# Performance work log

Measured on AMD Instinct MI355X. Metric: run time of the kernel, lower is better.

## Reference

```python
import jax, jax.numpy as jnp
import numpy as np

B, S = 16, 128
P, M, H = 512, 64, 256
I = P + M            # LTC input dim = perception + metadata
U = 2 * H            # ncp_units = hidden_dim * 2
OUT = 64             # belief head output size
UNFOLDS = 6          # ncps LTC default ode_unfolds
HEADS = 4
DH = H // HEADS


def setup_inputs() -> dict:
    key = jax.random.key(0)
    ks = jax.random.split(key, 24)
    u = lambda k, sh, lo, hi: jax.random.uniform(k, sh, jnp.float32, lo, hi)
    sgn = lambda k, sh: jnp.where(jax.random.bernoulli(k, 0.5, sh), 1.0, -1.0).astype(jnp.float32)
    msk = lambda k, sh: jax.random.bernoulli(k, 0.6, sh).astype(jnp.float32)
    gl = lambda k, sh, s: jax.random.normal(k, sh, jnp.float32) * s
    return dict(
        x=jax.random.normal(ks[0], (B, S, I), jnp.float32),
        # ncps LTC affine input/output maps (init: w=1, b=0)
        input_w=jnp.ones((I,), jnp.float32), input_b=jnp.zeros((I,), jnp.float32),
        # LTC cell params, ncps init ranges
        gleak=u(ks[1], (U,), 0.001, 1.0), vleak=u(ks[2], (U,), -0.2, 0.2),
        cm=u(ks[3], (U,), 0.4, 0.6),
        sigma=u(ks[4], (U, U), 3.0, 8.0), mu=u(ks[5], (U, U), 0.3, 0.8),
        w=u(ks[6], (U, U), 0.001, 1.0), erev=sgn(ks[7], (U, U)),
        sparsity_mask=msk(ks[8], (U, U)),  # AutoNCP sparse wiring surrogate
        sensory_sigma=u(ks[9], (I, U), 3.0, 8.0), sensory_mu=u(ks[10], (I, U), 0.3, 0.8),
        sensory_w=u(ks[11], (I, U), 0.001, 1.0), sensory_erev=sgn(ks[12], (I, U)),
        sensory_sparsity_mask=msk(ks[13], (I, U)),
        output_w=jnp.ones((H,), jnp.float32), output_b=jnp.zeros((H,), jnp.float32),
        # Hopfield (multi-head associative retrieval) projections
        Wq=gl(ks[14], (H, H), H ** -0.5), bq=jnp.zeros((H,), jnp.float32),
        Wk=gl(ks[15], (H, H), H ** -0.5), bk=jnp.zeros((H,), jnp.float32),
        Wv=gl(ks[16], (H, H), H ** -0.5), bv=jnp.zeros((H,), jnp.float32),
        Wo=gl(ks[17], (H, H), H ** -0.5), bo=jnp.zeros((H,), jnp.float32),
        # belief head
        W1=gl(ks[18], (H, H), H ** -0.5), b1=jnp.zeros((H,), jnp.float32),
        W2=gl(ks[19], (H, OUT), H ** -0.5), b2=jnp.zeros((OUT,), jnp.float32),
    )


def reference(x, input_w, input_b, gleak, vleak, cm, sigma, mu, w, erev,
              sparsity_mask, sensory_sigma, sensory_mu, sensory_w, sensory_erev,
              sensory_sparsity_mask, output_w, output_b,
              Wq, bq, Wk, bk, Wv, bv, Wo, bo, W1, b1, W2, b2):
    cm_t = cm * UNFOLDS  # cm / (elapsed_time / ode_unfolds), elapsed_time = 1.0

    @jax.checkpoint
    def cell(h, x_t):
        inp = x_t * input_w + input_b  # affine input map
        # sensory synapse activations: (B, I, U)
        sa = sensory_w * jax.nn.sigmoid(sensory_sigma * (inp[:, :, None] - sensory_mu)) * sensory_sparsity_mask
        w_num_s = jnp.sum(sa * sensory_erev, axis=1)  # (B, U)
        w_den_s = jnp.sum(sa, axis=1)
        v = h
        for _ in range(UNFOLDS):  # semi-implicit Euler ODE unfolds
            act = w * jax.nn.sigmoid(sigma * (v[:, :, None] - mu)) * sparsity_mask  # (B, U, U)
            w_num = jnp.sum(act * erev, axis=1) + w_num_s
            w_den = jnp.sum(act, axis=1) + w_den_s
            v = (cm_t * v + gleak * vleak + w_num) / (cm_t + gleak + w_den + 1e-8)
        out = v[:, :H] * output_w + output_b  # motor neurons + affine output map
        return v, out

    h0 = jnp.zeros((x.shape[0], U), x.dtype)
    h, outs = jax.lax.scan(cell, h0, jnp.swapaxes(x, 0, 1))  # outs: (S, B, H)
    ltc_out = jnp.swapaxes(outs, 0, 1)  # (B, S, H)

    # Hopfield associative memory (single update step == MHA self-retrieval)
    q = (ltc_out @ Wq + bq).reshape(B, S, HEADS, DH)
    k = (ltc_out @ Wk + bk).reshape(B, S, HEADS, DH)
    v = (ltc_out @ Wv + bv).reshape(B, S, HEADS, DH)
    attn = jax.nn.softmax(jnp.einsum('bqhd,bkhd->bhqk', q, k) / np.sqrt(DH).astype(np.float32), axis=-1)
    mem = jnp.einsum('bhqk,bkhd->bqhd', attn, v).reshape(B, S, H) @ Wo + bo

    combined = ltc_out + mem
    belief = jax.nn.silu(combined @ W1 + b1) @ W2 + b2
    return combined, belief, h
```

## Files before the change

### kernel.cpp

```cpp
#include <hip/hip_runtime.h>
#include <hip/hip_fp16.h>

#define L2E 1.4426950408889634f

constexpr int Bb = 16, Ss = 128, Ii = 576, Uu = 512, Hh = 256;

constexpr int OFF_AC   = 0;
constexpr int OFF_W2   = 262144;
constexpr int OFF_NUMS = 393216;
constexpr int OFF_DENS = 1441792;
constexpr int OFF_LTC  = 2499072;
constexpr int OFF_Q    = 3023360;
constexpr int OFF_K    = 3547648;
constexpr int OFF_V    = 4071936;
constexpr int OFF_MEM  = 4596224;
constexpr int OFF_HID  = 5120512;

constexpr unsigned SENT_U = 0x7FBADBADu;

__device__ __forceinline__ float ex2(float x) { return __builtin_amdgcn_exp2f(x); }
__device__ __forceinline__ float rcpf(float x) { return __builtin_amdgcn_rcpf(x); }

__global__ __launch_bounds__(256) void prep_kernel(
    const float* __restrict__ sigma, const float* __restrict__ mu,
    const float* __restrict__ w, const float* __restrict__ erev,
    const float* __restrict__ mask, float* __restrict__ ws)
{
    const int t = threadIdx.x;
    {
        const int g = blockIdx.x * 256 + t;
        if (g < 16 * 8 * 512) {
            const int r = (g >> 9) & 7;
            ws[OFF_HID + g] = (r == 7) ? 0.0f : __builtin_bit_cast(float, SENT_U);
        }
    }
    const int p = blockIdx.x * 256 + t;
    const int i2 = p >> 9, jj = p & 511;
    const int slice = jj >> 4, jl = jj & 15;
    unsigned* AC = (unsigned*)ws + OFF_AC;
    unsigned* W2 = (unsigned*)ws + OFF_W2;
    __half weh0, weh1;
    {
        const int i = i2 * 2;
        const int idx = i * 512 + jj;
        const float sg = sigma[idx], m = mu[idx];
        const float wm = w[idx] * mask[idx];
        __half2 ac; ac.x = __float2half_rn(sg * L2E); ac.y = __float2half_rn(sg * m * L2E);
        AC[slice * 8192 + ((i * 16 + jl) ^ (((i >> 5) & 1) << 4))] = __builtin_bit_cast(unsigned, ac);
        weh0 = __float2half_rn(wm * erev[idx]);
    }
    {
        const int i = i2 * 2 + 1;
        const int idx = i * 512 + jj;
        const float sg = sigma[idx], m = mu[idx];
        const float wm = w[idx] * mask[idx];
        __half2 ac; ac.x = __float2half_rn(sg * L2E); ac.y = __float2half_rn(sg * m * L2E);
        AC[slice * 8192 + ((i * 16 + jl) ^ (((i >> 5) & 1) << 4))] = __builtin_bit_cast(unsigned, ac);
        weh1 = __float2half_rn(wm * erev[idx]);
    }
    __half2 wp; wp.x = weh0; wp.y = weh1;
    W2[slice * 4096 + ((i2 * 16 + jl) ^ (((i2 >> 4) & 1) << 4))] = __builtin_bit_cast(unsigned, wp);
}

__global__ __launch_bounds__(256) void sensory_kernel(
    const float* __restrict__ x, const float* __restrict__ inw, const float* __restrict__ inb,
    const float* __restrict__ ssig, const float* __restrict__ smu,
    const float* __restrict__ sw, const float* __restrict__ serev,
    const float* __restrict__ smask, float* __restrict__ ws)
{
    __shared__ float inp[16 * 576];
    __shared__ float part[4096];
    const int t = threadIdx.x;
    const int jb = blockIdx.x & 7, pb = blockIdx.x >> 3;
    #pragma unroll
    for (int e = 0; e < 9; ++e) {
        const int id = t + e * 256;
        const int off = id * 4;
        const int bs = off / 576, ii = off % 576;
        const float4 xv = *(const float4*)&x[(pb * 16 + bs) * 576 + ii];
        const float4 wv = *(const float4*)&inw[ii];
        const float4 bv = *(const float4*)&inb[ii];
        inp[off + 0] = fmaf(xv.x, wv.x, bv.x);
        inp[off + 1] = fmaf(xv.y, wv.y, bv.y);
        inp[off + 2] = fmaf(xv.z, wv.z, bv.z);
        inp[off + 3] = fmaf(xv.w, wv.w, bv.w);
    }
    __syncthreads();
    const int j = t & 63, c = t >> 6;
    const int jg = jb * 64 + j;
    float num[16], den[16];
    #pragma unroll
    for (int bs = 0; bs < 16; ++bs) { num[bs] = 0.f; den[bs] = 0.f; }
    for (int ii = c * 144; ii < (c + 1) * 144; ++ii) {
        const int pidx = ii * 512 + jg;
        const float sg = ssig[pidx], m = smu[pidx];
        const float wm = sw[pidx] * smask[pidx];
        const float we = wm * serev[pidx];
        const float a = sg * L2E, cc = sg * m * L2E;
        #pragma unroll
        for (int bs = 0; bs < 16; ++bs) {
            const float vv = inp[bs * 576 + ii];
            const float r = rcpf(1.f + ex2(fmaf(-a, vv, cc)));
            num[bs] = fmaf(we, r, num[bs]);
            den[bs] = fmaf(wm, r, den[bs]);
        }
    }
    #pragma unroll
    for (int pass = 0; pass < 2; ++pass) {
        __syncthreads();
        #pragma unroll
        for (int bs = 0; bs < 8; ++bs) {
            part[((c * 64 + j) * 8 + bs) * 2 + 0] = num[pass * 8 + bs];
            part[((c * 64 + j) * 8 + bs) * 2 + 1] = den[pass * 8 + bs];
        }
        __syncthreads();
        #pragma unroll
        for (int qd = 0; qd < 4; ++qd) {
            const int vid = t * 4 + qd;
            const int jj2 = vid >> 4, bs = (vid >> 1) & 7, which = vid & 1;
            const float acc =
                part[((0 * 64 + jj2) * 8 + bs) * 2 + which] + part[((1 * 64 + jj2) * 8 + bs) * 2 + which] +
                part[((2 * 64 + jj2) * 8 + bs) * 2 + which] + part[((3 * 64 + jj2) * 8 + bs) * 2 + which];
            const int p = pb * 16 + pass * 8 + bs;
            ws[(which ? OFF_DENS : OFF_NUMS) + p * 512 + jb * 64 + jj2] = acc;
        }
    }
}

__global__ __launch_bounds__(256) void scan_kernel(
    const float* __restrict__ gleak, const float* __restrict__ vleak,
    const float* __restrict__ cmv,
    const float* __restrict__ outw, const float* __restrict__ outb,
    float* __restrict__ ws, float* __restrict__ dout)
{
    __shared__ unsigned prmAC[8192];
    __shared__ unsigned prmW2[4096];
    __shared__ float vlds[512];
    __shared__ float2 red[64];

    const int t = threadIdx.x;
    const int wg = blockIdx.x;
    const int batch = wg & 15;
    const int slice = wg >> 4;
    const int jl = t & 15;
    const int chunk = t >> 4;
    const unsigned swz = (unsigned)((chunk & 1) << 4);

    {
        const uint4* sA = (const uint4*)((const unsigned*)ws + OFF_AC) + slice * 2048;
        uint4* dA = (uint4*)prmAC;
        #pragma unroll
        for (int k = 0; k < 8; ++k) dA[t + k * 256] = sA[t + k * 256];
        const uint4* sW = (const uint4*)((const unsigned*)ws + OFF_W2) + slice * 1024;
        uint4* dW = (uint4*)prmW2;
        #pragma unroll
        for (int k = 0; k < 4; ++k) dW[t + k * 256] = sW[t + k * 256];
    }

    const bool owner = (t < 16);
    const int j = slice * 16 + jl;
    float gl = 0.f, glvl = 0.f, cmt = 0.f, ow = 0.f, ob = 0.f, vown = 0.f, sn = 0.f, sd = 0.f;
    if (owner) {
        gl = gleak[j]; glvl = gl * vleak[j]; cmt = cmv[j] * 6.f;
        if (j < Hh) { ow = outw[j]; ob = outb[j]; }
    }
    float* vb2 = ws + OFF_HID + batch * 4096;
    const float* snb = ws + OFF_NUMS + batch * (Ss * Uu);
    const float* sdb = ws + OFF_DENS + batch * (Ss * Uu);
    float* ltc = ws + OFF_LTC;

    __syncthreads();

    unsigned phase = 0;
    const int ibase = chunk * 32;

    for (int step = 0; step < Ss; ++step) {
        if (owner) { sn = snb[step * Uu + j]; sd = sdb[step * Uu + j]; }
        for (int uf = 0; uf < 6; ++uf) {
            if (owner) {
                __hip_atomic_store(vb2 + (((phase + 4) & 7) << 9) + j,
                                   __builtin_bit_cast(float, SENT_U),
                                   __ATOMIC_RELAXED, __HIP_MEMORY_SCOPE_AGENT);
            }
            {
                const float* src = vb2 + (((phase + 7) & 7) << 9);
                float va = 0.f, vc = 0.f;
                unsigned ua = SENT_U, uc = SENT_U;
                do {
                    if (ua == SENT_U) {
                        va = __hip_atomic_load(src + t, __ATOMIC_RELAXED, __HIP_MEMORY_SCOPE_AGENT);
                        ua = __builtin_bit_cast(unsigned, va);
                    }
                    if (uc == SENT_U) {
                        vc = __hip_atomic_load(src + t + 256, __ATOMIC_RELAXED, __HIP_MEMORY_SCOPE_AGENT);
                        uc = __builtin_bit_cast(unsigned, vc);
                    }
                } while (ua == SENT_U || uc == SENT_U);
                vlds[t] = va; vlds[t + 256] = vc;
            }
            __syncthreads();

            float n0 = 0.f, n1 = 0.f, d0 = 0.f, d1 = 0.f;
            #pragma unroll
            for (int kk = 0; kk < 8; ++kk) {
                const int ib = ibase + kk * 4;
                const float4 v4 = *(const float4*)&vlds[ib];
                const int eb = ib * 16 + jl;
                const int pbi = (ib >> 1) * 16 + jl;
                const unsigned ac0 = prmAC[(unsigned)(eb) ^ swz];
                const unsigned ac1 = prmAC[(unsigned)(eb + 16) ^ swz];
                const unsigned ac2 = prmAC[(unsigned)(eb + 32) ^ swz];
                const unsigned ac3 = prmAC[(unsigned)(eb + 48) ^ swz];
                const unsigned wp0 = prmW2[(unsigned)(pbi) ^ swz];
                const unsigned wp1 = prmW2[(unsigned)(pbi + 16) ^ swz];
                const float2 w01 = __half22float2(__builtin_bit_cast(__half2, wp0));
                const float2 w23 = __half22float2(__builtin_bit_cast(__half2, wp1));
                {
                    const float2 ac = __half22float2(__builtin_bit_cast(__half2, ac0));
                    const float r = rcpf(1.f + ex2(fmaf(-ac.x, v4.x, ac.y)));
                    n0 = fmaf(w01.x, r, n0); d0 = fmaf(fabsf(w01.x), r, d0);
                }
                {
                    const float2 ac = __half22float2(__builtin_bit_cast(__half2, ac1));
                    const float r = rcpf(1.f + ex2(fmaf(-ac.x, v4.y, ac.y)));
                    n1 = fmaf(w01.y, r, n1); d1 = fmaf(fabsf(w01.y), r, d1);
                }
                {
                    const float2 ac = __half22float2(__builtin_bit_cast(__half2, ac2));
                    const float r = rcpf(1.f + ex2(fmaf(-ac.x, v4.z, ac.y)));
                    n0 = fmaf(w23.x, r, n0); d0 = fmaf(fabsf(w23.x), r, d0);
                }
                {
                    const float2 ac = __half22float2(__builtin_bit_cast(__half2, ac3));
                    const float r = rcpf(1.f + ex2(fmaf(-ac.x, v4.w, ac.y)));
                    n1 = fmaf(w23.y, r, n1); d1 = fmaf(fabsf(w23.y), r, d1);
                }
            }
            float num = n0 + n1, den = d0 + d1;
            num += __shfl_xor(num, 16, 64); den += __shfl_xor(den, 16, 64);
            num += __shfl_xor(num, 32, 64); den += __shfl_xor(den, 32, 64);
            const int lane = t & 63, wave = t >> 6;
            if (lane < 16) red[wave * 16 + lane] = make_float2(num, den);
            __syncthreads();
            if (owner) {
                float rn = sn, rd = sd;
                #pragma unroll
                for (int wv = 0; wv < 4; ++wv) { const float2 pp = red[wv * 16 + t]; rn += pp.x; rd += pp.y; }
                const float vnew = (fmaf(cmt, vown, glvl) + rn) * rcpf(cmt + gl + rd + 1e-8f);
                vown = vnew;
                __hip_atomic_store(vb2 + ((phase & 7) << 9) + j, vnew,
                                   __ATOMIC_RELAXED, __HIP_MEMORY_SCOPE_AGENT);
            }
            ++phase;
        }
        if (owner && j < Hh) ltc[(batch * Ss + step) * Hh + j] = fmaf(vown, ow, ob);
    }
    if (owner) dout[524288 + 131072 + batch * Uu + j] = vown;
}

template <int MODE>
__global__ __launch_bounds__(256) void gemm_kernel(
    const float* __restrict__ A, const float* __restrict__ W,
    const float* __restrict__ bias, const float* __restrict__ R,
    float* __restrict__ C, const int N, const float scale)
{
    __shared__ float As[16][64];
    __shared__ float Bs[16][64];
    const int t = threadIdx.x;
    const int tx = t & 15, ty = t >> 4;
    const int by = blockIdx.x, bx = blockIdx.y;
    float acc[4][4] = {{0.f}};
    constexpr int K = 256;
    for (int k0 = 0; k0 < K; k0 += 16) {
        {
            const int r = t >> 2, c4 = (t & 3) << 2;
            const float4 a4 = *(const float4*)&A[(by * 64 + r) * K + k0 + c4];
            As[c4 + 0][r] = a4.x; As[c4 + 1][r] = a4.y; As[c4 + 2][r] = a4.z; As[c4 + 3][r] = a4.w;
        }
        {
            const int r = t >> 4, c4 = (t & 15) << 2;
            *(float4*)&Bs[r][c4] = *(const float4*)&W[(k0 + r) * N + bx * 64 + c4];
        }
        __syncthreads();
        #pragma unroll
        for (int kk = 0; kk < 16; ++kk) {
            const float4 a4 = *(const float4*)&As[kk][ty << 2];
            const float4 b4 = *(const float4*)&Bs[kk][tx << 2];
            acc[0][0] = fmaf(a4.x, b4.x, acc[0][0]); acc[0][1] = fmaf(a4.x, b4.y, acc[0][1]);
            acc[0][2] = fmaf(a4.x, b4.z, acc[0][2]); acc[0][3] = fmaf(a4.x, b4.w, acc[0][3]);
            acc[1][0] = fmaf(a4.y, b4.x, acc[1][0]); acc[1][1] = fmaf(a4.y, b4.y, acc[1][1]);
            acc[1][2] = fmaf(a4.y, b4.z, acc[1][2]); acc[1][3] = fmaf(a4.y, b4.w, acc[1][3]);
            acc[2][0] = fmaf(a4.z, b4.x, acc[2][0]); acc[2][1] = fmaf(a4.z, b4.y, acc[2][1]);
            acc[2][2] = fmaf(a4.z, b4.z, acc[2][2]); acc[2][3] = fmaf(a4.z, b4.w, acc[2][3]);
            acc[3][0] = fmaf(a4.w, b4.x, acc[3][0]); acc[3][1] = fmaf(a4.w, b4.y, acc[3][1]);
            acc[3][2] = fmaf(a4.w, b4.z, acc[3][2]); acc[3][3] = fmaf(a4.w, b4.w, acc[3][3]);
        }
        __syncthreads();
    }
    const int n0 = bx * 64 + (tx << 2);
    const float4 bv = *(const float4*)&bias[n0];
    #pragma unroll
    for (int i2 = 0; i2 < 4; ++i2) {
        const int m = by * 64 + (ty << 2) + i2;
        float4 o;
        o.x = acc[i2][0] + bv.x; o.y = acc[i2][1] + bv.y;
        o.z = acc[i2][2] + bv.z; o.w = acc[i2][3] + bv.w;
        if (MODE == 1) {
            o.x *= scale; o.y *= scale; o.z *= scale; o.w *= scale;
            const int b = m >> 7, s = m & 127;
            const int h = n0 >> 6, d = n0 & 63;
            *(float4*)&C[((b * 4 + h) * 128 + s) * 64 + d] = o;
        } else if (MODE == 2) {
            const float4 rv = *(const float4*)&R[m * N + n0];
            o.x += rv.x; o.y += rv.y; o.z += rv.z; o.w += rv.w;
            *(float4*)&C[m * N + n0] = o;
        } else if (MODE == 3) {
            o.x = o.x * rcpf(1.f + ex2(-o.x * L2E));
            o.y = o.y * rcpf(1.f + ex2(-o.y * L2E));
            o.z = o.z * rcpf(1.f + ex2(-o.z * L2E));
            o.w = o.w * rcpf(1.f + ex2(-o.w * L2E));
            *(float4*)&C[m * N + n0] = o;
        } else {
            *(float4*)&C[m * N + n0] = o;
        }
    }
}

__global__ __launch_bounds__(256) void attn_kernel(
    const float* __restrict__ q, const float* __restrict__ k,
    const float* __restrict__ v, float* __restrict__ mem)
{
    __shared__ float KV[128 * 66];
    __shared__ float Qs[16 * 66];
    __shared__ float P[16 * 128];
    const int t = threadIdx.x;
    const int qb = blockIdx.x & 7;
    const int bh = blockIdx.x >> 3;
    const float* qp = q + bh * (128 * 64);
    const float* kp = k + bh * (128 * 64);
    const float* vp = v + bh * (128 * 64);
    {
        const int r = t >> 4, d4 = (t & 15) << 2;
        const float4 x4 = *(const float4*)&qp[(qb * 16 + r) * 64 + d4];
        Qs[r * 66 + d4 + 0] = x4.x; Qs[r * 66 + d4 + 1] = x4.y;
        Qs[r * 66 + d4 + 2] = x4.z; Qs[r * 66 + d4 + 3] = x4.w;
    }
    #pragma unroll
    for (int e = 0; e < 8; ++e) {
        const int id = t + e * 256;
        const int s = id >> 4, d4 = (id & 15) << 2;
        const float4 x4 = *(const float4*)&kp[s * 64 + d4];
        KV[s * 66 + d4 + 0] = x4.x; KV[s * 66 + d4 + 1] = x4.y;
        KV[s * 66 + d4 + 2] = x4.z; KV[s * 66 + d4 + 3] = x4.w;
    }
    __syncthreads();
    const int qi = t >> 4, sc = t & 15;
    float pv[8];
    float mx = -3.4e38f;
    #pragma unroll
    for (int s8 = 0; s8 < 8; ++s8) {
        const int s = s8 * 16 + sc;
        float dot = 0.f;
        #pragma unroll
        for (int d4 = 0; d4 < 16; ++d4) {
            const float4 qv = *(const float4*)&Qs[qi * 66 + d4 * 4];
            const float4 kv = *(const float4*)&KV[s * 66 + d4 * 4];
            dot = fmaf(qv.x, kv.x, dot); dot = fmaf(qv.y, kv.y, dot);
            dot = fmaf(qv.z, kv.z, dot); dot = fmaf(qv.w, kv.w, dot);
        }
        pv[s8] = dot;
        mx = fmaxf(mx, dot);
    }
    #pragma unroll
    for (int off = 1; off < 16; off <<= 1) mx = fmaxf(mx, __shfl_xor(mx, off, 16));
    float sum = 0.f;
    #pragma unroll
    for (int s8 = 0; s8 < 8; ++s8) {
        const int s = s8 * 16 + sc;
        const float p = ex2((pv[s8] - mx) * L2E);
        P[qi * 128 + s] = p;
        sum += p;
    }
    #pragma unroll
    for (int off = 1; off < 16; off <<= 1) sum += __shfl_xor(sum, off, 16);
    const float inv = rcpf(sum);
    __syncthreads();
    #pragma unroll
    for (int e = 0; e < 8; ++e) {
        const int id = t + e * 256;
        const int s = id >> 4, d4 = (id & 15) << 2;
        *(float4*)&KV[s * 64 + d4] = *(const float4*)&vp[s * 64 + d4];
    }
    __syncthreads();
    float4 acc = {0.f, 0.f, 0.f, 0.f};
    for (int s = 0; s < 128; ++s) {
        const float p = P[qi * 128 + s];
        const float4 v4 = *(const float4*)&KV[s * 64 + (sc << 2)];
        acc.x = fmaf(p, v4.x, acc.x); acc.y = fmaf(p, v4.y, acc.y);
        acc.z = fmaf(p, v4.z, acc.z); acc.w = fmaf(p, v4.w, acc.w);
    }
    acc.x *= inv; acc.y *= inv; acc.z *= inv; acc.w *= inv;
    const int b = bh >> 2, h = bh & 3;
    const int m = b * 128 + qb * 16 + qi;
    *(float4*)&mem[m * 256 + h * 64 + (sc << 2)] = acc;
}

extern "C" void kernel_launch(void* const* d_in, const int* in_sizes, int n_in,
                              void* d_out, int out_size, void* d_ws, size_t ws_size,
                              hipStream_t stream)
{
    const float* x     = (const float*)d_in[0];
    const float* inw   = (const float*)d_in[1];
    const float* inb   = (const float*)d_in[2];
    const float* gleak = (const float*)d_in[3];
    const float* vleak = (const float*)d_in[4];
    const float* cm    = (const float*)d_in[5];
    const float* sigma = (const float*)d_in[6];
    const float* mu    = (const float*)d_in[7];
    const float* w     = (const float*)d_in[8];
    const float* erev  = (const float*)d_in[9];
    const float* maskr = (const float*)d_in[10];
    const float* ssig  = (const float*)d_in[11];
    const float* smu   = (const float*)d_in[12];
    const float* sw    = (const float*)d_in[13];
    const float* serev = (const float*)d_in[14];
    const float* smask = (const float*)d_in[15];
    const float* outw  = (const float*)d_in[16];
    const float* outb  = (const float*)d_in[17];
    const float* Wq    = (const float*)d_in[18];
    const float* bq    = (const float*)d_in[19];
    const float* Wk    = (const float*)d_in[20];
    const float* bk    = (const float*)d_in[21];
    const float* Wv    = (const float*)d_in[22];
    const float* bv    = (const float*)d_in[23];
    const float* Wo    = (const float*)d_in[24];
    const float* bo    = (const float*)d_in[25];
    const float* W1    = (const float*)d_in[26];
    const float* b1    = (const float*)d_in[27];
    const float* W2    = (const float*)d_in[28];
    const float* b2    = (const float*)d_in[29];

    float* ws  = (float*)d_ws;
    float* out = (float*)d_out;

    prep_kernel<<<512, 256, 0, stream>>>(sigma, mu, w, erev, maskr, ws);
    sensory_kernel<<<1024, 256, 0, stream>>>(x, inw, inb, ssig, smu, sw, serev, smask, ws);
    scan_kernel<<<512, 256, 0, stream>>>(gleak, vleak, cm, outw, outb, ws, out);

    dim3 gA(32, 4);
    gemm_kernel<1><<<gA, 256, 0, stream>>>(ws + OFF_LTC, Wq, bq, nullptr, ws + OFF_Q, 256, 0.125f);
    gemm_kernel<1><<<gA, 256, 0, stream>>>(ws + OFF_LTC, Wk, bk, nullptr, ws + OFF_K, 256, 1.f);
    gemm_kernel<1><<<gA, 256, 0, stream>>>(ws + OFF_LTC, Wv, bv, nullptr, ws + OFF_V, 256, 1.f);
    attn_kernel<<<512, 256, 0, stream>>>(ws + OFF_Q, ws + OFF_K, ws + OFF_V, ws + OFF_MEM);
    gemm_kernel<2><<<gA, 256, 0, stream>>>(ws + OFF_MEM, Wo, bo, ws + OFF_LTC, out, 256, 1.f);
    gemm_kernel<3><<<gA, 256, 0, stream>>>(out, W1, b1, nullptr, ws + OFF_HID, 256, 1.f);
    dim3 gB(32, 1);
    gemm_kernel<0><<<gB, 256, 0, stream>>>(ws + OFF_HID, W2, b2, nullptr, out + 524288, 64, 1.f);
}
```

Before: 2.168 ms.

## Hold LTC cell parameters in registers and reduce per-column within a wave

The scan kernel no longer copies the sigma/mu and weight tables into shared memory. Each thread now keeps its 32 packed (a,c) pairs and 16 packed weights in registers, and the prep kernel lays the tables out column-major so those loads are contiguous. Each 16-lane group owns one output neuron and reduces entirely through wave shuffles, which removes the second __syncthreads and the shared reduction array from every unfold. The v buffer is double-buffered and swizzled to cut bank conflicts. The cost is higher register pressure per thread.

```diff
diff --git a/kernel.cpp b/kernel.cpp
--- a/kernel.cpp
+++ b/kernel.cpp
@@ -27,39 +27,27 @@
     const float* __restrict__ mask, float* __restrict__ ws)
 {
     const int t = threadIdx.x;
-    {
-        const int g = blockIdx.x * 256 + t;
-        if (g < 16 * 8 * 512) {
-            const int r = (g >> 9) & 7;
-            ws[OFF_HID + g] = (r == 7) ? 0.0f : __builtin_bit_cast(float, SENT_U);
-        }
-    }
-    const int p = blockIdx.x * 256 + t;
-    const int i2 = p >> 9, jj = p & 511;
-    const int slice = jj >> 4, jl = jj & 15;
+    const int g = blockIdx.x * 256 + t;
+    if (g < 16 * 8 * 512) {
+        const int r = (g >> 9) & 7;
+        ws[OFF_HID + g] = (r == 7) ? 0.0f : __builtin_bit_cast(float, SENT_U);
+    }
+    const int j = g >> 8;
+    const int p = g & 255;
+    const int i0 = p * 2, i1 = p * 2 + 1;
     unsigned* AC = (unsigned*)ws + OFF_AC;
     unsigned* W2 = (unsigned*)ws + OFF_W2;
-    __half weh0, weh1;
-    {
-        const int i = i2 * 2;
-        const int idx = i * 512 + jj;
-        const float sg = sigma[idx], m = mu[idx];
-        const float wm = w[idx] * mask[idx];
-        __half2 ac; ac.x = __float2half_rn(sg * L2E); ac.y = __float2half_rn(sg * m * L2E);
-        AC[slice * 8192 + ((i * 16 + jl) ^ (((i >> 5) & 1) << 4))] = __builtin_bit_cast(unsigned, ac);
-        weh0 = __float2half_rn(wm * erev[idx]);
-    }
-    {
-        const int i = i2 * 2 + 1;
-        const int idx = i * 512 + jj;
-        const float sg = sigma[idx], m = mu[idx];
-        const float wm = w[idx] * mask[idx];
-        __half2 ac; ac.x = __float2half_rn(sg * L2E); ac.y = __float2half_rn(sg * m * L2E);
-        AC[slice * 8192 + ((i * 16 + jl) ^ (((i >> 5) & 1) << 4))] = __builtin_bit_cast(unsigned, ac);
-        weh1 = __float2half_rn(wm * erev[idx]);
-    }
-    __half2 wp; wp.x = weh0; wp.y = weh1;
-    W2[slice * 4096 + ((i2 * 16 + jl) ^ (((i2 >> 4) & 1) << 4))] = __builtin_bit_cast(unsigned, wp);
+    const int x0 = i0 * 512 + j, x1 = i1 * 512 + j;
+    const float sg0 = sigma[x0], m0 = mu[x0];
+    const float wm0 = w[x0] * mask[x0], we0 = wm0 * erev[x0];
+    const float sg1 = sigma[x1], m1 = mu[x1];
+    const float wm1 = w[x1] * mask[x1], we1 = wm1 * erev[x1];
+    __half2 ac0; ac0.x = __float2half_rn(sg0 * L2E); ac0.y = __float2half_rn(sg0 * m0 * L2E);
+    __half2 ac1; ac1.x = __float2half_rn(sg1 * L2E); ac1.y = __float2half_rn(sg1 * m1 * L2E);
+    AC[j * 512 + i0] = __builtin_bit_cast(unsigned, ac0);
+    AC[j * 512 + i1] = __builtin_bit_cast(unsigned, ac1);
+    __half2 wp; wp.x = __float2half_rn(we0); wp.y = __float2half_rn(we1);
+    W2[j * 256 + p] = __builtin_bit_cast(unsigned, wp);
 }
 
 __global__ __launch_bounds__(256) void sensory_kernel(
@@ -133,57 +121,59 @@
     const float* __restrict__ outw, const float* __restrict__ outb,
     float* __restrict__ ws, float* __restrict__ dout)
 {
-    __shared__ unsigned prmAC[8192];
-    __shared__ unsigned prmW2[4096];
-    __shared__ float vlds[512];
-    __shared__ float2 red[64];
+    __shared__ float vlds[2][512];
 
     const int t = threadIdx.x;
     const int wg = blockIdx.x;
     const int batch = wg & 15;
     const int slice = wg >> 4;
-    const int jl = t & 15;
-    const int chunk = t >> 4;
-    const unsigned swz = (unsigned)((chunk & 1) << 4);
-
+    const int lane = t & 63;
+    const int wv = t >> 6;
+    const int colL = lane >> 4;
+    const int rg = lane & 15;
+    const int j = slice * 16 + wv * 4 + colL;
+    const bool owner = (rg == 0);
+
+    unsigned ac[32], wep[16];
     {
-        const uint4* sA = (const uint4*)((const unsigned*)ws + OFF_AC) + slice * 2048;
-        uint4* dA = (uint4*)prmAC;
-        #pragma unroll
-        for (int k = 0; k < 8; ++k) dA[t + k * 256] = sA[t + k * 256];
-        const uint4* sW = (const uint4*)((const unsigned*)ws + OFF_W2) + slice * 1024;
-        uint4* dW = (uint4*)prmW2;
-        #pragma unroll
-        for (int k = 0; k < 4; ++k) dW[t + k * 256] = sW[t + k * 256];
-    }
-
-    const bool owner = (t < 16);
-    const int j = slice * 16 + jl;
+        const unsigned* ACg = (const unsigned*)ws + OFF_AC + j * 512 + rg * 32;
+        #pragma unroll
+        for (int q = 0; q < 8; ++q) {
+            const uint4 u = ((const uint4*)ACg)[q];
+            ac[q * 4 + 0] = u.x; ac[q * 4 + 1] = u.y; ac[q * 4 + 2] = u.z; ac[q * 4 + 3] = u.w;
+        }
+        const unsigned* WEg = (const unsigned*)ws + OFF_W2 + j * 256 + rg * 16;
+        #pragma unroll
+        for (int q = 0; q < 4; ++q) {
+            const uint4 u = ((const uint4*)WEg)[q];
+            wep[q * 4 + 0] = u.x; wep[q * 4 + 1] = u.y; wep[q * 4 + 2] = u.z; wep[q * 4 + 3] = u.w;
+        }
+    }
     float gl = 0.f, glvl = 0.f, cmt = 0.f, ow = 0.f, ob = 0.f, vown = 0.f, sn = 0.f, sd = 0.f;
     if (owner) {
         gl = gleak[j]; glvl = gl * vleak[j]; cmt = cmv[j] * 6.f;
         if (j < Hh) { ow = outw[j]; ob = outb[j]; }
     }
-    float* vb2 = ws + OFF_HID + batch * 4096;
+    float* ring = ws + OFF_HID + batch * 4096;
     const float* snb = ws + OFF_NUMS + batch * (Ss * Uu);
     const float* sdb = ws + OFF_DENS + batch * (Ss * Uu);
     float* ltc = ws + OFF_LTC;
 
-    __syncthreads();
+    const int sw0 = t ^ (((t >> 5) & 7) << 2);
 
     unsigned phase = 0;
-    const int ibase = chunk * 32;
+    int buf = 0;
 
     for (int step = 0; step < Ss; ++step) {
         if (owner) { sn = snb[step * Uu + j]; sd = sdb[step * Uu + j]; }
         for (int uf = 0; uf < 6; ++uf) {
             if (owner) {
-                __hip_atomic_store(vb2 + (((phase + 4) & 7) << 9) + j,
+                __hip_atomic_store(ring + (((phase + 4) & 7) << 9) + j,
                                    __builtin_bit_cast(float, SENT_U),
                                    __ATOMIC_RELAXED, __HIP_MEMORY_SCOPE_AGENT);
             }
             {
-                const float* src = vb2 + (((phase + 7) & 7) << 9);
+                const float* src = ring + (((phase + 7) & 7) << 9);
                 float va = 0.f, vc = 0.f;
                 unsigned ua = SENT_U, uc = SENT_U;
                 do {
@@ -196,62 +186,44 @@
                         uc = __builtin_bit_cast(unsigned, vc);
                     }
                 } while (ua == SENT_U || uc == SENT_U);
-                vlds[t] = va; vlds[t + 256] = vc;
+                vlds[buf][sw0] = va; vlds[buf][sw0 + 256] = vc;
             }
             __syncthreads();
 
             float n0 = 0.f, n1 = 0.f, d0 = 0.f, d1 = 0.f;
+            const float* vb = vlds[buf];
+            float2 wef = make_float2(0.f, 0.f);
             #pragma unroll
-            for (int kk = 0; kk < 8; ++kk) {
-                const int ib = ibase + kk * 4;
-                const float4 v4 = *(const float4*)&vlds[ib];
-                const int eb = ib * 16 + jl;
-                const int pbi = (ib >> 1) * 16 + jl;
-                const unsigned ac0 = prmAC[(unsigned)(eb) ^ swz];
-                const unsigned ac1 = prmAC[(unsigned)(eb + 16) ^ swz];
-                const unsigned ac2 = prmAC[(unsigned)(eb + 32) ^ swz];
-                const unsigned ac3 = prmAC[(unsigned)(eb + 48) ^ swz];
-                const unsigned wp0 = prmW2[(unsigned)(pbi) ^ swz];
-                const unsigned wp1 = prmW2[(unsigned)(pbi + 16) ^ swz];
-                const float2 w01 = __half22float2(__builtin_bit_cast(__half2, wp0));
-                const float2 w23 = __half22float2(__builtin_bit_cast(__half2, wp1));
-                {
-                    const float2 ac = __half22float2(__builtin_bit_cast(__half2, ac0));
-                    const float r = rcpf(1.f + ex2(fmaf(-ac.x, v4.x, ac.y)));
-                    n0 = fmaf(w01.x, r, n0); d0 = fmaf(fabsf(w01.x), r, d0);
-                }
-                {
-                    const float2 ac = __half22float2(__builtin_bit_cast(__half2, ac1));
-                    const float r = rcpf(1.f + ex2(fmaf(-ac.x, v4.y, ac.y)));
-                    n1 = fmaf(w01.y, r, n1); d1 = fmaf(fabsf(w01.y), r, d1);
-                }
-                {
-                    const float2 ac = __half22float2(__builtin_bit_cast(__half2, ac2));
-                    const float r = rcpf(1.f + ex2(fmaf(-ac.x, v4.z, ac.y)));
-                    n0 = fmaf(w23.x, r, n0); d0 = fmaf(fabsf(w23.x), r, d0);
-                }
-                {
-                    const float2 ac = __half22float2(__builtin_bit_cast(__half2, ac3));
-                    const float r = rcpf(1.f + ex2(fmaf(-ac.x, v4.w, ac.y)));
-                    n1 = fmaf(w23.y, r, n1); d1 = fmaf(fabsf(w23.y), r, d1);
+            for (int k4 = 0; k4 < 8; ++k4) {
+                const int idx = (rg * 32 + k4 * 4) ^ ((rg & 7) << 2);
+                const float4 v4 = *(const float4*)&vb[idx];
+                #pragma unroll
+                for (int kk = 0; kk < 4; ++kk) {
+                    const int k = k4 * 4 + kk;
+                    const float vi = (kk == 0) ? v4.x : (kk == 1) ? v4.y : (kk == 2) ? v4.z : v4.w;
+                    const float2 a = __half22float2(__builtin_bit_cast(__half2, ac[k]));
+                    const float r = rcpf(1.f + ex2(fmaf(-a.x, vi, a.y)));
+                    if ((k & 1) == 0) {
+                        wef = __half22float2(__builtin_bit_cast(__half2, wep[k >> 1]));
+                        n0 = fmaf(wef.x, r, n0); d0 = fmaf(fabsf(wef.x), r, d0);
+                    } else {
+                        n1 = fmaf(wef.y, r, n1); d1 = fmaf(fabsf(wef.y), r, d1);
+                    }
                 }
             }
-            float num = n0 + n1, den = d0 + d1;
-            num += __shfl_xor(num, 16, 64); den += __shfl_xor(den, 16, 64);
-            num += __shfl_xor(num, 32, 64); den += __shfl_xor(den, 32, 64);
-            const int lane = t & 63, wave = t >> 6;
-            if (lane < 16) red[wave * 16 + lane] = make_float2(num, den);
-            __syncthreads();
+            float n = n0 + n1, d = d0 + d1;
+            n += __shfl_xor(n, 1, 64); d += __shfl_xor(d, 1, 64);
+            n += __shfl_xor(n, 2, 64); d += __shfl_xor(d, 2, 64);
+            n += __shfl_xor(n, 4, 64); d += __shfl_xor(d, 4, 64);
+            n += __shfl_xor(n, 8, 64); d += __shfl_xor(d, 8, 64);
             if (owner) {
-                float rn = sn, rd = sd;
-                #pragma unroll
-                for (int wv = 0; wv < 4; ++wv) { const float2 pp = red[wv * 16 + t]; rn += pp.x; rd += pp.y; }
+                const float rn = n + sn, rd = d + sd;
                 const float vnew = (fmaf(cmt, vown, glvl) + rn) * rcpf(cmt + gl + rd + 1e-8f);
                 vown = vnew;
-                __hip_atomic_store(vb2 + ((phase & 7) << 9) + j, vnew,
+                __hip_atomic_store(ring + ((phase & 7) << 9) + j, vnew,
                                    __ATOMIC_RELAXED, __HIP_MEMORY_SCOPE_AGENT);
             }
-            ++phase;
+            ++phase; buf ^= 1;
         }
         if (owner && j < Hh) ltc[(batch * Ss + step) * Hh + j] = fmaf(vown, ow, ob);
     }
```

Measured after the change: 2.139 ms. Within noise of the previous version (-1.3%).
